# Performance work log

Measured on AMD Instinct MI355X. Metric: run time of the kernel, lower is better.

Reference implementation:

```python
import jax, jax.numpy as jnp
import numpy as np

L, B = 64, 8
BITS = np.array([2, 3, 4, 5, 6, 7, 8, 16], dtype=np.float32)
DENOM = (2.0 ** BITS - 1.0)  # (1<<b) - 1 per candidate bitwidth
EPS = 0.02
ITERS = 200


def setup_inputs() -> dict:
    key = jax.random.key(0)
    k0, k1, k2, k3, k4 = jax.random.split(key, 5)
    theta = jax.random.normal(k0, (L, B), dtype=jnp.float32) * 0.01
    phi = jax.random.normal(k1, (B,), dtype=jnp.float32) * 0.1
    trH = jax.random.uniform(k2, (L,), dtype=jnp.float32, minval=0.5, maxval=2.0)
    wmax = jax.random.uniform(k3, (L,), dtype=jnp.float32, minval=0.1, maxval=1.0)
    sizes = jax.random.uniform(k4, (L,), dtype=jnp.float32, minval=0.5, maxval=1.5)
    a = sizes / sizes.sum()  # a = n / n.sum() as in __init__
    return {"theta": theta, "phi": phi, "trH": trH, "wmax": wmax, "a": a}


def reference(theta, phi, trH, wmax, a):
    denom = jnp.asarray(DENOM)                       # [B]
    # build_cost: C = 0.5 * trH * (2*wmax/denom)^2 / 12
    delta = 2.0 * wmax[:, None] / denom[None, :]      # [L,B]
    C = 0.5 * trH[:, None] * (delta * delta / 12.0)   # [L,B]
    cost = C - theta                                  # compute_P passes C - theta
    K = -cost / EPS                                   # [L,B]
    b = jax.nn.softmax(phi)                           # self.b()
    log_a = jnp.log(a + 1e-40)
    log_b = jnp.log(b + 1e-40)

    def step(carry, _):
        f, g = carry
        f = log_a - jax.nn.logsumexp(K + g[None, :], axis=1)  # row update [L]
        g = log_b - jax.nn.logsumexp(K + f[:, None], axis=0)  # col update [B]
        return (f, g), None

    init = (jnp.zeros((L,), jnp.float32), jnp.zeros((B,), jnp.float32))
    (f, g), _ = jax.lax.scan(step, init, None, length=ITERS)

    P = jnp.exp(K + f[:, None] + g[None, :])
    return P / (P.sum() + 1e-40)
```

## Files before the change

kernel.cpp:

```cpp
#include <hip/hip_runtime.h>

#define NITERS 200

template<int CTRL>
__device__ __forceinline__ float dpp_add(float v) {
    int y = __builtin_amdgcn_mov_dpp(__float_as_int(v), CTRL, 0xF, 0xF, true);
    return v + __int_as_float(y);
}

#if __has_builtin(__builtin_amdgcn_permlane16_swap)
__device__ __forceinline__ float xor16_add(float v) {
    unsigned u = __float_as_uint(v);
    auto r = __builtin_amdgcn_permlane16_swap(u, u, false, false);
    return __uint_as_float(r[0]) + __uint_as_float(r[1]);
}
#else
__device__ __forceinline__ float xor16_add(float v) { return v + __shfl_xor(v, 16, 64); }
#endif

#if __has_builtin(__builtin_amdgcn_permlane32_swap)
__device__ __forceinline__ float xor32_add(float v) {
    unsigned u = __float_as_uint(v);
    auto r = __builtin_amdgcn_permlane32_swap(u, u, false, false);
    return __uint_as_float(r[0]) + __uint_as_float(r[1]);
}
#else
__device__ __forceinline__ float xor32_add(float v) { return v + __shfl_xor(v, 32, 64); }
#endif

__global__ __launch_bounds__(64)
void sinkhorn64x8(const float* __restrict__ theta,
                  const float* __restrict__ phi,
                  const float* __restrict__ trH,
                  const float* __restrict__ wmax,
                  const float* __restrict__ a,
                  float* __restrict__ out)
{
    const int lane = threadIdx.x & 63;
    const int j = lane & 7;
    const int r = lane >> 3;
    const int l0 = r * 8;

    const float denomj = (j == 7) ? 65535.0f : (float)((1u << (j + 2)) - 1u);
    const float inv_den = 1.0f / denomj;

    float ph[8];
#pragma unroll
    for (int k = 0; k < 8; ++k) ph[k] = phi[k];
    float mx = ph[0];
#pragma unroll
    for (int k = 1; k < 8; ++k) mx = fmaxf(mx, ph[k]);
    float es = 0.0f, ee[8];
#pragma unroll
    for (int k = 0; k < 8; ++k) { ee[k] = expf(ph[k] - mx); es += ee[k]; }
    const float B = ee[j] / es + 1e-40f;

    float E[8], EA[8];
#pragma unroll
    for (int i = 0; i < 8; ++i) {
        const int l = l0 + i;
        const float w = wmax[l];
        const float d = 2.0f * w * inv_den;
        const float C = 0.5f * trH[l] * (d * d * (1.0f / 12.0f));
        const float K = (theta[l * 8 + j] - C) / 0.02f;
        E[i] = expf(K);
        EA[i] = E[i] * (a[l] + 1e-40f);
    }

    float rinv[8];
    float G = 1.0f;

#pragma unroll 2
    for (int it = 0; it < NITERS; ++it) {
        float p[8];
#pragma unroll
        for (int i = 0; i < 8; ++i) p[i] = E[i] * G;
#pragma unroll
        for (int i = 0; i < 8; ++i) {
            p[i] = dpp_add<0xB1>(p[i]);
            p[i] = dpp_add<0x4E>(p[i]);
            p[i] = dpp_add<0x141>(p[i]);
        }
#pragma unroll
        for (int i = 0; i < 8; ++i) rinv[i] = __builtin_amdgcn_rcpf(p[i]);

        const float q01 = EA[0] * rinv[0] + EA[1] * rinv[1];
        const float q23 = EA[2] * rinv[2] + EA[3] * rinv[3];
        const float q45 = EA[4] * rinv[4] + EA[5] * rinv[5];
        const float q67 = EA[6] * rinv[6] + EA[7] * rinv[7];
        float q = (q01 + q23) + (q45 + q67);
        q = dpp_add<0x128>(q);
        q = xor16_add(q);
        q = xor32_add(q);
        G = B * __builtin_amdgcn_rcpf(q);
    }

    float P[8];
#pragma unroll
    for (int i = 0; i < 8; ++i) P[i] = EA[i] * rinv[i] * G;
    float t = ((P[0] + P[1]) + (P[2] + P[3])) + ((P[4] + P[5]) + (P[6] + P[7]));
    t = dpp_add<0xB1>(t);
    t = dpp_add<0x4E>(t);
    t = dpp_add<0x141>(t);
    t = dpp_add<0x128>(t);
    t = xor16_add(t);
    t = xor32_add(t);
    const float inv = 1.0f / (t + 1e-40f);
#pragma unroll
    for (int i = 0; i < 8; ++i) out[(l0 + i) * 8 + j] = P[i] * inv;
}

extern "C" void kernel_launch(void* const* d_in, const int* in_sizes, int n_in,
                              void* d_out, int out_size, void* d_ws, size_t ws_size,
                              hipStream_t stream) {
    const float* theta = (const float*)d_in[0];
    const float* phi   = (const float*)d_in[1];
    const float* trH   = (const float*)d_in[2];
    const float* wmax  = (const float*)d_in[3];
    const float* a     = (const float*)d_in[4];
    float* out = (float*)d_out;
    sinkhorn64x8<<<dim3(1), dim3(64), 0, stream>>>(theta, phi, trH, wmax, a, out);
}
```

Baseline: 91.49 us.

## Replace per-row butterfly reductions with a transposed XOR-indexed reduce-scatter

```diff
diff --git a/kernel.cpp b/kernel.cpp
--- a/kernel.cpp
+++ b/kernel.cpp
@@ -3,10 +3,19 @@
 #define NITERS 200
 
 template<int CTRL>
-__device__ __forceinline__ float dpp_add(float v) {
-    int y = __builtin_amdgcn_mov_dpp(__float_as_int(v), CTRL, 0xF, 0xF, true);
-    return v + __int_as_float(y);
+__device__ __forceinline__ float dpp_mov(float v) {
+    return __int_as_float(
+        __builtin_amdgcn_mov_dpp(__float_as_int(v), CTRL, 0xF, 0xF, true));
 }
+template<int CTRL>
+__device__ __forceinline__ float dpp_add(float a, float b) {
+    return a + dpp_mov<CTRL>(b);
+}
+
+#define XOR1 0xB1
+#define XOR2 0x4E
+#define MIR7 0x141
+#define XOR8 0x128
 
 #if __has_builtin(__builtin_amdgcn_permlane16_swap)
 __device__ __forceinline__ float xor16_add(float v) {
@@ -17,7 +26,6 @@
 #else
 __device__ __forceinline__ float xor16_add(float v) { return v + __shfl_xor(v, 16, 64); }
 #endif
-
 #if __has_builtin(__builtin_amdgcn_permlane32_swap)
 __device__ __forceinline__ float xor32_add(float v) {
     unsigned u = __float_as_uint(v);
@@ -58,7 +66,7 @@
     float E[8], EA[8];
 #pragma unroll
     for (int i = 0; i < 8; ++i) {
-        const int l = l0 + i;
+        const int l = l0 + (j ^ i);
         const float w = wmax[l];
         const float d = 2.0f * w * inv_den;
         const float C = 0.5f * trH[l] * (d * d * (1.0f / 12.0f));
@@ -67,29 +75,38 @@
         EA[i] = E[i] * (a[l] + 1e-40f);
     }
 
-    float rinv[8];
+    float rv[8];
+#pragma unroll
+    for (int i = 0; i < 8; ++i) rv[i] = 0.0f;
     float G = 1.0f;
 
-#pragma unroll 2
     for (int it = 0; it < NITERS; ++it) {
-        float p[8];
-#pragma unroll
-        for (int i = 0; i < 8; ++i) p[i] = E[i] * G;
-#pragma unroll
-        for (int i = 0; i < 8; ++i) {
-            p[i] = dpp_add<0xB1>(p[i]);
-            p[i] = dpp_add<0x4E>(p[i]);
-            p[i] = dpp_add<0x141>(p[i]);
-        }
-#pragma unroll
-        for (int i = 0; i < 8; ++i) rinv[i] = __builtin_amdgcn_rcpf(p[i]);
+        float x0 = E[0] * G, x1 = E[1] * G, x2 = E[2] * G, x3 = E[3] * G;
+        float x4 = E[4] * G, x5 = E[5] * G, x6 = E[6] * G, x7 = E[7] * G;
+        const float s0 = dpp_add<XOR1>(x0, x1);
+        const float s2 = dpp_add<XOR1>(x2, x3);
+        const float s5 = dpp_add<XOR1>(x5, x4);
+        const float s7 = dpp_add<XOR1>(x7, x6);
+        const float t0 = dpp_add<XOR2>(s0, s2);
+        const float t7 = dpp_add<XOR2>(s7, s5);
+        const float p  = dpp_add<MIR7>(t0, t7);
+        const float rinv = __builtin_amdgcn_rcpf(p);
 
-        const float q01 = EA[0] * rinv[0] + EA[1] * rinv[1];
-        const float q23 = EA[2] * rinv[2] + EA[3] * rinv[3];
-        const float q45 = EA[4] * rinv[4] + EA[5] * rinv[5];
-        const float q67 = EA[6] * rinv[6] + EA[7] * rinv[7];
+        rv[0] = rinv;
+        rv[1] = dpp_mov<XOR1>(rv[0]);
+        rv[2] = dpp_mov<XOR2>(rv[0]);
+        rv[3] = dpp_mov<XOR2>(rv[1]);
+        rv[7] = dpp_mov<MIR7>(rv[0]);
+        rv[6] = dpp_mov<MIR7>(rv[1]);
+        rv[5] = dpp_mov<MIR7>(rv[2]);
+        rv[4] = dpp_mov<MIR7>(rv[3]);
+
+        const float q01 = EA[0] * rv[0] + EA[1] * rv[1];
+        const float q23 = EA[2] * rv[2] + EA[3] * rv[3];
+        const float q45 = EA[4] * rv[4] + EA[5] * rv[5];
+        const float q67 = EA[6] * rv[6] + EA[7] * rv[7];
         float q = (q01 + q23) + (q45 + q67);
-        q = dpp_add<0x128>(q);
+        q = dpp_add<XOR8>(q, q);
         q = xor16_add(q);
         q = xor32_add(q);
         G = B * __builtin_amdgcn_rcpf(q);
@@ -97,17 +114,18 @@
 
     float P[8];
 #pragma unroll
-    for (int i = 0; i < 8; ++i) P[i] = EA[i] * rinv[i] * G;
+    for (int i = 0; i < 8; ++i) P[i] = EA[i] * rv[i] * G;
     float t = ((P[0] + P[1]) + (P[2] + P[3])) + ((P[4] + P[5]) + (P[6] + P[7]));
-    t = dpp_add<0xB1>(t);
-    t = dpp_add<0x4E>(t);
-    t = dpp_add<0x141>(t);
-    t = dpp_add<0x128>(t);
+    t = dpp_add<XOR1>(t, t);
+    t = dpp_add<XOR2>(t, t);
+    t = dpp_add<MIR7>(t, t);
+    t = dpp_add<XOR8>(t, t);
     t = xor16_add(t);
     t = xor32_add(t);
     const float inv = 1.0f / (t + 1e-40f);
 #pragma unroll
-    for (int i = 0; i < 8; ++i) out[(l0 + i) * 8 + j] = P[i] * inv;
+    for (int i = 0; i < 8; ++i)
+        out[(l0 + (j ^ i)) * 8 + j] = P[i] * inv;
 }
 
 extern "C" void kernel_launch(void* const* d_in, const int* in_sizes, int n_in,
```

Result: faster. 82.66 us (-9.7%).
